# Optimization experiments

Measured on AMD Instinct MI355X. Metric: run time of the kernel, lower is better.

## Reference

```python
import jax, jax.numpy as jnp
import numpy as np

N_GROUPS = 32
N_HEADS = 8
EPS = 1e-5


def group_norm(x, w, b):
    # x: [B, C, T]; GroupNorm32 computes in fp32 then casts back
    B, C, T = x.shape
    xf = x.astype(jnp.float32).reshape(B, N_GROUPS, (C // N_GROUPS) * T)
    mean = xf.mean(axis=-1, keepdims=True)
    var = xf.var(axis=-1, keepdims=True)
    xn = ((xf - mean) * jax.lax.rsqrt(var + EPS)).reshape(B, C, T)
    return (xn * w[None, :, None] + b[None, :, None]).astype(x.dtype)


def attention_block(x, norm_w, norm_b, qkv_w, qkv_b, proj_w, proj_b):
    B, C = x.shape[0], x.shape[1]
    spatial = x.shape[2:]
    xr = x.reshape(B, C, -1)  # [B, C, T]
    T = xr.shape[-1]
    h = group_norm(xr, norm_w, norm_b)
    # 1x1 Conv1d == per-position matmul: [B, 3C, T]
    qkv = jnp.einsum('oc,bct->bot', qkv_w, h) + qkv_b[None, :, None]
    ch = C // N_HEADS  # per-head channels
    q, k, v = jnp.split(qkv, 3, axis=1)
    q = q.reshape(B * N_HEADS, ch, T)
    k = k.reshape(B * N_HEADS, ch, T)
    v = v.reshape(B * N_HEADS, ch, T)
    scale = 1.0 / np.sqrt(ch)
    w = jnp.einsum('bct,bcs->bts', q * scale, k)  # [B*H, T, T]
    w = jax.nn.softmax(w.astype(jnp.float32), axis=-1).astype(w.dtype)
    a = jnp.einsum('bts,bcs->bct', w, v).reshape(B, C, T)
    a = jnp.einsum('oc,bct->bot', proj_w, a) + proj_b[None, :, None]
    return (xr + a).reshape(B, C, *spatial)


def setup_inputs() -> dict:
    key = jax.random.key(0)
    ks = jax.random.split(key, 6)
    B, C, H, W = 16, 512, 32, 32
    return {
        'x': jax.random.normal(ks[0], (B, C, H, W), jnp.float32),
        'norm_w': jnp.ones((C,), jnp.float32),
        'norm_b': jnp.zeros((C,), jnp.float32),
        'qkv_w': jax.random.normal(ks[1], (3 * C, C), jnp.float32) * (1.0 / np.sqrt(C)),
        'qkv_b': jax.random.normal(ks[2], (3 * C,), jnp.float32) * 0.02,
        'proj_w': jax.random.normal(ks[3], (C, C), jnp.float32) * (1.0 / np.sqrt(C)),
        'proj_b': jax.random.normal(ks[4], (C,), jnp.float32) * 0.02,
    }


def reference(x, norm_w, norm_b, qkv_w, qkv_b, proj_w, proj_b):
    return attention_block(x, norm_w, norm_b, qkv_w, qkv_b, proj_w, proj_b)
```

## Files before the change

kernel.cpp:

```cpp
#include <hip/hip_runtime.h>
#include <hip/hip_bf16.h>

#define B_ 16
#define C_ 512
#define T_ 1024
#define G_ 32
#define CPG 16
#define NH 8
#define CH 64
#define EPS 1e-5f

typedef __bf16 bf16x8 __attribute__((ext_vector_type(8)));
typedef __bf16 bf16x4 __attribute__((ext_vector_type(4)));
typedef float f32x4 __attribute__((ext_vector_type(4)));
typedef float f32x16 __attribute__((ext_vector_type(16)));
typedef int i32x4 __attribute__((ext_vector_type(4)));

__device__ __forceinline__ void gload16(const __bf16* g, const __bf16* l) {
    __builtin_amdgcn_global_load_lds(
        (const __attribute__((address_space(1))) unsigned int*)(unsigned long long)(uintptr_t)g,
        (__attribute__((address_space(3))) unsigned int*)(unsigned int)(uintptr_t)l,
        16, 0, 0);
}

__global__ __launch_bounds__(256) void convw_kernel(const float* __restrict__ qw,
                                                    const float* __restrict__ pw,
                                                    __bf16* __restrict__ wqb,
                                                    __bf16* __restrict__ wpb) {
    int idx = (blockIdx.x * 256 + threadIdx.x) * 8;
    const float* src;
    __bf16* dst;
    if (idx < 1536 * 512) { src = qw + idx; dst = wqb + idx; }
    else { src = pw + (idx - 1536 * 512); dst = wpb + (idx - 1536 * 512); }
    float4 a = *(const float4*)src, b = *(const float4*)(src + 4);
    bf16x8 t;
    t[0] = (__bf16)a.x; t[1] = (__bf16)a.y; t[2] = (__bf16)a.z; t[3] = (__bf16)a.w;
    t[4] = (__bf16)b.x; t[5] = (__bf16)b.y; t[6] = (__bf16)b.z; t[7] = (__bf16)b.w;
    *(bf16x8*)dst = t;
}

__global__ __launch_bounds__(256) void gn_kernel(const float* __restrict__ x,
                                                 const float* __restrict__ w,
                                                 const float* __restrict__ bvec,
                                                 __bf16* __restrict__ h_t) {
    const int blk = blockIdx.x;
    const int bb = blk >> 5;
    const int g  = blk & 31;
    const size_t base = ((size_t)bb * C_ + (size_t)g * CPG) * T_;
    const float4* xp = (const float4*)(x + base);
    float4 vals[16];
    float s = 0.f, sq = 0.f;
#pragma unroll
    for (int i = 0; i < 16; ++i) {
        float4 v = xp[threadIdx.x + i * 256];
        vals[i] = v;
        s  += v.x + v.y + v.z + v.w;
        sq += v.x * v.x + v.y * v.y + v.z * v.z + v.w * v.w;
    }
#pragma unroll
    for (int off = 32; off > 0; off >>= 1) {
        s  += __shfl_down(s, off);
        sq += __shfl_down(sq, off);
    }
    __shared__ float red[2][4];
    const int lane = threadIdx.x & 63, wid = threadIdx.x >> 6;
    if (lane == 0) { red[0][wid] = s; red[1][wid] = sq; }
    __syncthreads();
    s  = red[0][0] + red[0][1] + red[0][2] + red[0][3];
    sq = red[1][0] + red[1][1] + red[1][2] + red[1][3];
    const float mean = s * (1.f / 16384.f);
    const float var  = sq * (1.f / 16384.f) - mean * mean;
    const float rstd = rsqrtf(var + EPS);
    float scv[16], shv[16];
#pragma unroll
    for (int i = 0; i < 16; ++i) {
        scv[i] = w[g * CPG + i] * rstd;
        shv[i] = bvec[g * CPG + i] - mean * scv[i];
    }
    __bf16* hb = h_t + ((size_t)bb * T_ + 4 * threadIdx.x) * C_ + g * CPG;
#pragma unroll
    for (int j = 0; j < 4; ++j) {
        bf16x8 t0, t1;
#pragma unroll
        for (int i = 0; i < 8; ++i) {
            float f0 = ((const float*)&vals[i])[j];
            float f1 = ((const float*)&vals[i + 8])[j];
            t0[i] = (__bf16)(f0 * scv[i] + shv[i]);
            t1[i] = (__bf16)(f1 * scv[i + 8] + shv[i + 8]);
        }
        *(bf16x8*)(hb + (size_t)j * C_) = t0;
        *(bf16x8*)(hb + (size_t)j * C_ + 8) = t1;
    }
}

template<int MODE>
__global__ __launch_bounds__(256) void gemm_mfma(const __bf16* __restrict__ Wb,
                                                 const float* __restrict__ bias,
                                                 const __bf16* __restrict__ Bin,
                                                 const float* __restrict__ xres,
                                                 __bf16* __restrict__ qt,
                                                 __bf16* __restrict__ kt,
                                                 __bf16* __restrict__ vb,
                                                 float* __restrict__ outp) {
    __shared__ __align__(16) __bf16 smem[18432];
    __bf16* As = smem;
    __bf16* Bt = smem + 8192;
    const int tid = threadIdx.x, lane = tid & 63, wv = tid >> 6;
    const int wr = wv >> 1, wc = wv & 1, frow = lane & 15, fgrp = lane >> 4;
    const int bz = blockIdx.z, o0 = blockIdx.y << 7, t0 = blockIdx.x << 7;
    const int lrow = lane >> 3, lblk = (lane & 7) ^ (lrow & 7);

    const __bf16* gA = Wb + (size_t)(o0 + wv * 32 + lrow) * 512 + lblk * 8;
    const __bf16* gB = Bin + ((size_t)bz * T_ + t0 + wv * 32 + lrow) * 512 + lblk * 8;
    __bf16* lA = As + wv * 32 * 64;
    __bf16* lB = Bt + wv * 32 * 64;
    const int sb0 = (fgrp ^ (frow & 7)) * 8;
    const int sb1 = ((4 + fgrp) ^ (frow & 7)) * 8;

    f32x4 acc[4][4] = {};
    for (int k0 = 0; k0 < 512; k0 += 64) {
#pragma unroll
        for (int j = 0; j < 4; ++j) {
            gload16(gA + j * 4096 + k0, lA + j * 512);
            gload16(gB + j * 4096 + k0, lB + j * 512);
        }
        __syncthreads();
        bf16x8 af[4][2], bfr[4][2];
#pragma unroll
        for (int m = 0; m < 4; ++m) {
            const __bf16* r = As + (wr * 64 + m * 16 + frow) * 64;
            af[m][0] = *(const bf16x8*)(r + sb0);
            af[m][1] = *(const bf16x8*)(r + sb1);
        }
#pragma unroll
        for (int n = 0; n < 4; ++n) {
            const __bf16* r = Bt + (wc * 64 + n * 16 + frow) * 64;
            bfr[n][0] = *(const bf16x8*)(r + sb0);
            bfr[n][1] = *(const bf16x8*)(r + sb1);
        }
#pragma unroll
        for (int kk = 0; kk < 2; ++kk)
#pragma unroll
            for (int m = 0; m < 4; ++m)
#pragma unroll
                for (int n = 0; n < 4; ++n)
                    acc[m][n] = __builtin_amdgcn_mfma_f32_16x16x32_bf16(af[m][kk], bfr[n][kk], acc[m][n], 0, 0, 0);
        __syncthreads();
    }

    float bias_v[4][4];
#pragma unroll
    for (int m = 0; m < 4; ++m)
#pragma unroll
        for (int r = 0; r < 4; ++r)
            bias_v[m][r] = bias[o0 + wr * 64 + m * 16 + fgrp * 4 + r];

    __bf16* e = smem + wv * 4608;
    if (MODE == 0 && o0 < 1024) {
        const float qsc = (o0 < 512) ? 0.18033688f : 1.0f;
#pragma unroll
        for (int m = 0; m < 4; ++m)
#pragma unroll
            for (int n = 0; n < 4; ++n) {
                bf16x4 v;
#pragma unroll
                for (int r = 0; r < 4; ++r) v[r] = (__bf16)((acc[m][n][r] + bias_v[m][r]) * qsc);
                *(bf16x4*)&e[(n * 16 + frow) * 72 + m * 16 + fgrp * 4] = v;
            }
        __syncthreads();
        __bf16* dst = (o0 < 512) ? qt : kt;
        const int ob = o0 & 511;
#pragma unroll
        for (int p = 0; p < 8; ++p) {
            int row = p * 8 + (lane >> 3), c8 = (lane & 7) * 8;
            *(bf16x8*)(dst + ((size_t)bz * T_ + t0 + wc * 64 + row) * 512 + ob + wr * 64 + c8) =
                *(const bf16x8*)&e[row * 72 + c8];
        }
    } else {
#pragma unroll
        for (int m = 0; m < 4; ++m)
#pragma unroll
            for (int n = 0; n < 4; ++n)
#pragma unroll
                for (int r = 0; r < 4; ++r)
                    e[(m * 16 + fgrp * 4 + r) * 72 + n * 16 + frow] =
                        (__bf16)(acc[m][n][r] + bias_v[m][r]);
        __syncthreads();
        if (MODE == 0) {
            const int ob = o0 - 1024;
#pragma unroll
            for (int p = 0; p < 8; ++p) {
                int row = p * 8 + (lane >> 3), c8 = (lane & 7) * 8;
                *(bf16x8*)(vb + ((size_t)bz * C_ + ob + wr * 64 + row) * T_ + t0 + wc * 64 + c8) =
                    *(const bf16x8*)&e[row * 72 + c8];
            }
        } else {
#pragma unroll
            for (int p = 0; p < 8; ++p) {
                int row = p * 8 + (lane >> 3), c8 = (lane & 7) * 8;
                int o = o0 + wr * 64 + row;
                size_t base = ((size_t)bz * C_ + o) * T_ + t0 + wc * 64 + c8;
                bf16x8 v = *(const bf16x8*)&e[row * 72 + c8];
                float4 x0 = *(const float4*)(xres + base);
                float4 x1 = *(const float4*)(xres + base + 4);
                float4 r0, r1;
                r0.x = x0.x + (float)v[0]; r0.y = x0.y + (float)v[1];
                r0.z = x0.z + (float)v[2]; r0.w = x0.w + (float)v[3];
                r1.x = x1.x + (float)v[4]; r1.y = x1.y + (float)v[5];
                r1.z = x1.z + (float)v[6]; r1.w = x1.w + (float)v[7];
                *(float4*)(outp + base) = r0;
                *(float4*)(outp + base + 4) = r1;
            }
        }
    }
}

__global__ __launch_bounds__(256) void attn32_kernel(const __bf16* __restrict__ qt,
                                                     const __bf16* __restrict__ kt,
                                                     const __bf16* __restrict__ vbuf,
                                                     __bf16* __restrict__ aout) {
    __shared__ __align__(16) __bf16 smem[16384];
    const int tid = threadIdx.x, lane = tid & 63, wv = tid >> 6;
    const int ln = lane & 31, hi = lane >> 5;
    const int lin = blockIdx.y * 8 + blockIdx.x;
    const int work = (lin & 7) * 128 + (lin >> 3);
    const int head = work >> 3;
    const int bb = head >> 3, hh = head & 7;
    const int tq0 = (work & 7) << 7;

    const __bf16* qbase = qt + (size_t)bb * T_ * 512 + hh * CH;
    const __bf16* kbase = kt + (size_t)bb * T_ * 512 + hh * CH;
    const __bf16* vbase = vbuf + ((size_t)bb * C_ + hh * CH) * T_;

    bf16x8 qf[4];
    {
        const __bf16* qr = qbase + (size_t)(tq0 + wv * 32 + ln) * 512 + hi * 8;
#pragma unroll
        for (int st = 0; st < 4; ++st) qf[st] = *(const bf16x8*)(qr + st * 16);
    }

    const int r8 = lane >> 3, cbs = (lane & 7) ^ (lane >> 3);

    f32x16 o0_ = {}, o1_ = {};
    float l = 0.f;

    {
#pragma unroll
        for (int c = 0; c < 2; ++c) {
            int ch = wv * 2 + c;
            gload16(kbase + (size_t)(ch * 8 + r8) * 512 + cbs * 8, smem + ch * 512);
            gload16(vbase + (size_t)(ch * 8 + r8) * T_ + cbs * 8, smem + 4096 + ch * 512);
        }
    }
    __syncthreads();

#pragma unroll 2
    for (int it = 0; it < 16; ++it) {
        const int cur = it & 1;
        if (it < 15) {
            const int s0 = (it + 1) << 6;
            __bf16* base = smem + (cur ^ 1) * 8192;
#pragma unroll
            for (int c = 0; c < 2; ++c) {
                int ch = wv * 2 + c;
                gload16(kbase + (size_t)(s0 + ch * 8 + r8) * 512 + cbs * 8, base + ch * 512);
                gload16(vbase + (size_t)(ch * 8 + r8) * T_ + s0 + cbs * 8, base + 4096 + ch * 512);
            }
        }
        const __bf16* Kb = smem + cur * 8192;
        const __bf16* Vb = Kb + 4096;
        const int rx = ln & 7;

        f32x16 sa0 = {}, sa1 = {};
        {
            const __bf16* kr0 = Kb + (size_t)ln * 64;
            const __bf16* kr1 = Kb + (size_t)(32 + ln) * 64;
            __builtin_amdgcn_s_setprio(1);
#pragma unroll
            for (int st = 0; st < 4; ++st) {
                const int cb = ((hi + 2 * st) ^ rx) << 3;
                bf16x8 k0 = *(const bf16x8*)(kr0 + cb);
                bf16x8 k1 = *(const bf16x8*)(kr1 + cb);
                sa0 = __builtin_amdgcn_mfma_f32_32x32x16_bf16(k0, qf[st], sa0, 0, 0, 0);
                sa1 = __builtin_amdgcn_mfma_f32_32x32x16_bf16(k1, qf[st], sa1, 0, 0, 0);
            }
            __builtin_amdgcn_s_setprio(0);
        }

        float psum0 = 0.f, psum1 = 0.f;
#pragma unroll
        for (int i = 0; i < 16; ++i) {
            sa0[i] = __builtin_amdgcn_exp2f(sa0[i]); psum0 += sa0[i];
        }
#pragma unroll
        for (int i = 0; i < 16; ++i) {
            sa1[i] = __builtin_amdgcn_exp2f(sa1[i]); psum1 += sa1[i];
        }
        l += psum0 + psum1;

        unsigned Wd0[8], Wd1[8];
#pragma unroll
        for (int q = 0; q < 8; ++q) {
            unsigned a0 = (unsigned)__builtin_bit_cast(unsigned short, (__bf16)sa0[2 * q]);
            unsigned a1 = (unsigned)__builtin_bit_cast(unsigned short, (__bf16)sa0[2 * q + 1]);
            Wd0[q] = a0 | (a1 << 16);
            unsigned b0 = (unsigned)__builtin_bit_cast(unsigned short, (__bf16)sa1[2 * q]);
            unsigned b1 = (unsigned)__builtin_bit_cast(unsigned short, (__bf16)sa1[2 * q + 1]);
            Wd1[q] = b0 | (b1 << 16);
        }
        bf16x8 pf[4];
#pragma unroll
        for (int st = 0; st < 4; ++st) {
            const unsigned* W = (st >> 1) ? Wd1 : Wd0;
            const int hf = (st & 1) * 4;
            auto r02 = __builtin_amdgcn_permlane32_swap((int)W[hf + 0], (int)W[hf + 2], false, false);
            auto r13 = __builtin_amdgcn_permlane32_swap((int)W[hf + 1], (int)W[hf + 3], false, false);
            i32x4 pk;
            pk[0] = r02[0]; pk[1] = r13[0]; pk[2] = r02[1]; pk[3] = r13[1];
            pf[st] = __builtin_bit_cast(bf16x8, pk);
        }

        {
            const __bf16* vr0 = Vb + (size_t)ln * 64;
            const __bf16* vr1 = Vb + (size_t)(32 + ln) * 64;
            __builtin_amdgcn_s_setprio(1);
#pragma unroll
            for (int st = 0; st < 4; ++st) {
                const int cb = ((hi + 2 * st) ^ rx) << 3;
                bf16x8 v0 = *(const bf16x8*)(vr0 + cb);
                bf16x8 v1 = *(const bf16x8*)(vr1 + cb);
                o0_ = __builtin_amdgcn_mfma_f32_32x32x16_bf16(v0, pf[st], o0_, 0, 0, 0);
                o1_ = __builtin_amdgcn_mfma_f32_32x32x16_bf16(v1, pf[st], o1_, 0, 0, 0);
            }
            __builtin_amdgcn_s_setprio(0);
        }
        __syncthreads();
    }

    l += __shfl_xor(l, 32);
    const float rl = 1.f / l;
    __bf16* e = smem + wv * 2304;
#pragma unroll
    for (int ct = 0; ct < 2; ++ct) {
        const f32x16& oc = ct ? o1_ : o0_;
#pragma unroll
        for (int q = 0; q < 8; ++q) {
            int c0 = ct * 32 + 2 * (q & 1) + 8 * (q >> 1) + 4 * hi;
            unsigned u0 = (unsigned)__builtin_bit_cast(unsigned short, (__bf16)(oc[2 * q] * rl));
            unsigned u1 = (unsigned)__builtin_bit_cast(unsigned short, (__bf16)(oc[2 * q + 1] * rl));
            *(unsigned*)&e[(size_t)ln * 72 + c0] = u0 | (u1 << 16);
        }
    }
    __syncthreads();
    {
        const int t = lane >> 1, chalf = lane & 1;
        __bf16* dst = aout + ((size_t)bb * T_ + tq0 + wv * 32 + t) * 512 + hh * CH + chalf * 32;
        const __bf16* er = e + t * 72 + chalf * 32;
#pragma unroll
        for (int k = 0; k < 4; ++k)
            *(bf16x8*)(dst + k * 8) = *(const bf16x8*)(er + k * 8);
    }
}

extern "C" void kernel_launch(void* const* d_in, const int* in_sizes, int n_in,
                              void* d_out, int out_size, void* d_ws, size_t ws_size,
                              hipStream_t stream) {
    const float* x      = (const float*)d_in[0];
    const float* norm_w = (const float*)d_in[1];
    const float* norm_b = (const float*)d_in[2];
    const float* qkv_w  = (const float*)d_in[3];
    const float* qkv_b  = (const float*)d_in[4];
    const float* proj_w = (const float*)d_in[5];
    const float* proj_b = (const float*)d_in[6];
    float* out = (float*)d_out;

    __bf16* h_t = (__bf16*)d_ws;
    __bf16* wqb = h_t + (size_t)8388608;
    __bf16* wpb = wqb + 786432;
    __bf16* qt  = wpb + 262144;
    __bf16* kt  = qt + (size_t)8388608;
    __bf16* vb  = kt + (size_t)8388608;
    __bf16* at  = vb + (size_t)8388608;

    convw_kernel<<<512, 256, 0, stream>>>(qkv_w, proj_w, wqb, wpb);
    gn_kernel<<<512, 256, 0, stream>>>(x, norm_w, norm_b, h_t);
    gemm_mfma<0><<<dim3(8, 12, 16), 256, 0, stream>>>(wqb, qkv_b, h_t, nullptr, qt, kt, vb, nullptr);
    attn32_kernel<<<dim3(8, 128), 256, 0, stream>>>(qt, kt, vb, at);
    gemm_mfma<1><<<dim3(8, 4, 16), 256, 0, stream>>>(wpb, proj_b, at, x, nullptr, nullptr, nullptr, out);
}
```

Measured before the change: 123.0 us.

## Double query rows per wave in attention to reuse K/V tiles

Each wave now handles 64 query rows (two 32-row subtiles) instead of 32, so a block covers 256 queries and the grid shrinks from 1024 to 512 blocks. Each K and V fragment read from LDS feeds twice as many MFMAs, and K/V global traffic per query is halved. The cost is double the accumulator and score registers, which pressures occupancy, and fewer blocks on the GPU. Launch bounds are set to 2 blocks per CU and the epilogue staging buffer is enlarged to hold 256 rows.

Result: faster. 116.6 us (-5.2%).

```diff
diff --git a/kernel.cpp b/kernel.cpp
--- a/kernel.cpp
+++ b/kernel.cpp
@@ -215,42 +215,42 @@
     }
 }
 
-__global__ __launch_bounds__(256) void attn32_kernel(const __bf16* __restrict__ qt,
-                                                     const __bf16* __restrict__ kt,
-                                                     const __bf16* __restrict__ vbuf,
-                                                     __bf16* __restrict__ aout) {
-    __shared__ __align__(16) __bf16 smem[16384];
+__global__ __launch_bounds__(256, 2) void attn32_kernel(const __bf16* __restrict__ qt,
+                                                        const __bf16* __restrict__ kt,
+                                                        const __bf16* __restrict__ vbuf,
+                                                        __bf16* __restrict__ aout) {
+    __shared__ __align__(16) __bf16 smem[18432];
     const int tid = threadIdx.x, lane = tid & 63, wv = tid >> 6;
     const int ln = lane & 31, hi = lane >> 5;
-    const int lin = blockIdx.y * 8 + blockIdx.x;
-    const int work = (lin & 7) * 128 + (lin >> 3);
-    const int head = work >> 3;
+    const int lin = blockIdx.x;
+    const int work = (lin & 7) * 64 + (lin >> 3);
+    const int head = work >> 2;
     const int bb = head >> 3, hh = head & 7;
-    const int tq0 = (work & 7) << 7;
+    const int tq0 = (work & 3) << 8;
 
     const __bf16* qbase = qt + (size_t)bb * T_ * 512 + hh * CH;
     const __bf16* kbase = kt + (size_t)bb * T_ * 512 + hh * CH;
     const __bf16* vbase = vbuf + ((size_t)bb * C_ + hh * CH) * T_;
 
-    bf16x8 qf[4];
-    {
-        const __bf16* qr = qbase + (size_t)(tq0 + wv * 32 + ln) * 512 + hi * 8;
-#pragma unroll
-        for (int st = 0; st < 4; ++st) qf[st] = *(const bf16x8*)(qr + st * 16);
+    bf16x8 qf[2][4];
+#pragma unroll
+    for (int sub = 0; sub < 2; ++sub) {
+        const __bf16* qr = qbase + (size_t)(tq0 + wv * 64 + sub * 32 + ln) * 512 + hi * 8;
+#pragma unroll
+        for (int st = 0; st < 4; ++st) qf[sub][st] = *(const bf16x8*)(qr + st * 16);
     }
 
     const int r8 = lane >> 3, cbs = (lane & 7) ^ (lane >> 3);
-
-    f32x16 o0_ = {}, o1_ = {};
-    float l = 0.f;
-
-    {
-#pragma unroll
-        for (int c = 0; c < 2; ++c) {
-            int ch = wv * 2 + c;
-            gload16(kbase + (size_t)(ch * 8 + r8) * 512 + cbs * 8, smem + ch * 512);
-            gload16(vbase + (size_t)(ch * 8 + r8) * T_ + cbs * 8, smem + 4096 + ch * 512);
-        }
+    const int rx = ln & 7;
+
+    f32x16 o00 = {}, o01 = {}, o10 = {}, o11 = {};
+    float l0 = 0.f, l1 = 0.f;
+
+#pragma unroll
+    for (int c = 0; c < 2; ++c) {
+        int ch = wv * 2 + c;
+        gload16(kbase + (size_t)(ch * 8 + r8) * 512 + cbs * 8, smem + ch * 512);
+        gload16(vbase + (size_t)(ch * 8 + r8) * T_ + cbs * 8, smem + 4096 + ch * 512);
     }
     __syncthreads();
 
@@ -258,106 +258,118 @@
     for (int it = 0; it < 16; ++it) {
         const int cur = it & 1;
         if (it < 15) {
-            const int s0 = (it + 1) << 6;
+            const int s0n = (it + 1) << 6;
             __bf16* base = smem + (cur ^ 1) * 8192;
 #pragma unroll
             for (int c = 0; c < 2; ++c) {
                 int ch = wv * 2 + c;
-                gload16(kbase + (size_t)(s0 + ch * 8 + r8) * 512 + cbs * 8, base + ch * 512);
-                gload16(vbase + (size_t)(ch * 8 + r8) * T_ + s0 + cbs * 8, base + 4096 + ch * 512);
+                gload16(kbase + (size_t)(s0n + ch * 8 + r8) * 512 + cbs * 8, base + ch * 512);
+                gload16(vbase + (size_t)(ch * 8 + r8) * T_ + s0n + cbs * 8, base + 4096 + ch * 512);
             }
         }
         const __bf16* Kb = smem + cur * 8192;
         const __bf16* Vb = Kb + 4096;
-        const int rx = ln & 7;
-
-        f32x16 sa0 = {}, sa1 = {};
+
+        f32x16 sa00 = {}, sa01 = {}, sa10 = {}, sa11 = {};
         {
-            const __bf16* kr0 = Kb + (size_t)ln * 64;
-            const __bf16* kr1 = Kb + (size_t)(32 + ln) * 64;
             __builtin_amdgcn_s_setprio(1);
 #pragma unroll
             for (int st = 0; st < 4; ++st) {
                 const int cb = ((hi + 2 * st) ^ rx) << 3;
-                bf16x8 k0 = *(const bf16x8*)(kr0 + cb);
-                bf16x8 k1 = *(const bf16x8*)(kr1 + cb);
-                sa0 = __builtin_amdgcn_mfma_f32_32x32x16_bf16(k0, qf[st], sa0, 0, 0, 0);
-                sa1 = __builtin_amdgcn_mfma_f32_32x32x16_bf16(k1, qf[st], sa1, 0, 0, 0);
+                bf16x8 k0 = *(const bf16x8*)(Kb + (size_t)ln * 64 + cb);
+                bf16x8 k1 = *(const bf16x8*)(Kb + (size_t)(32 + ln) * 64 + cb);
+                sa00 = __builtin_amdgcn_mfma_f32_32x32x16_bf16(k0, qf[0][st], sa00, 0, 0, 0);
+                sa01 = __builtin_amdgcn_mfma_f32_32x32x16_bf16(k1, qf[0][st], sa01, 0, 0, 0);
+                sa10 = __builtin_amdgcn_mfma_f32_32x32x16_bf16(k0, qf[1][st], sa10, 0, 0, 0);
+                sa11 = __builtin_amdgcn_mfma_f32_32x32x16_bf16(k1, qf[1][st], sa11, 0, 0, 0);
             }
             __builtin_amdgcn_s_setprio(0);
         }
 
-        float psum0 = 0.f, psum1 = 0.f;
-#pragma unroll
-        for (int i = 0; i < 16; ++i) {
-            sa0[i] = __builtin_amdgcn_exp2f(sa0[i]); psum0 += sa0[i];
-        }
-#pragma unroll
-        for (int i = 0; i < 16; ++i) {
-            sa1[i] = __builtin_amdgcn_exp2f(sa1[i]); psum1 += sa1[i];
-        }
-        l += psum0 + psum1;
-
-        unsigned Wd0[8], Wd1[8];
-#pragma unroll
-        for (int q = 0; q < 8; ++q) {
-            unsigned a0 = (unsigned)__builtin_bit_cast(unsigned short, (__bf16)sa0[2 * q]);
-            unsigned a1 = (unsigned)__builtin_bit_cast(unsigned short, (__bf16)sa0[2 * q + 1]);
-            Wd0[q] = a0 | (a1 << 16);
-            unsigned b0 = (unsigned)__builtin_bit_cast(unsigned short, (__bf16)sa1[2 * q]);
-            unsigned b1 = (unsigned)__builtin_bit_cast(unsigned short, (__bf16)sa1[2 * q + 1]);
-            Wd1[q] = b0 | (b1 << 16);
-        }
-        bf16x8 pf[4];
-#pragma unroll
-        for (int st = 0; st < 4; ++st) {
-            const unsigned* W = (st >> 1) ? Wd1 : Wd0;
-            const int hf = (st & 1) * 4;
-            auto r02 = __builtin_amdgcn_permlane32_swap((int)W[hf + 0], (int)W[hf + 2], false, false);
-            auto r13 = __builtin_amdgcn_permlane32_swap((int)W[hf + 1], (int)W[hf + 3], false, false);
-            i32x4 pk;
-            pk[0] = r02[0]; pk[1] = r13[0]; pk[2] = r02[1]; pk[3] = r13[1];
-            pf[st] = __builtin_bit_cast(bf16x8, pk);
+        float pa = 0.f, pb = 0.f, pc = 0.f, pd = 0.f;
+#pragma unroll
+        for (int i = 0; i < 16; ++i) { sa00[i] = __builtin_amdgcn_exp2f(sa00[i]); pa += sa00[i]; }
+#pragma unroll
+        for (int i = 0; i < 16; ++i) { sa01[i] = __builtin_amdgcn_exp2f(sa01[i]); pb += sa01[i]; }
+#pragma unroll
+        for (int i = 0; i < 16; ++i) { sa10[i] = __builtin_amdgcn_exp2f(sa10[i]); pc += sa10[i]; }
+#pragma unroll
+        for (int i = 0; i < 16; ++i) { sa11[i] = __builtin_amdgcn_exp2f(sa11[i]); pd += sa11[i]; }
+        l0 += pa + pb;
+        l1 += pc + pd;
+
+        bf16x8 pfA[4], pfB[4];
+#pragma unroll
+        for (int sub = 0; sub < 2; ++sub) {
+            const f32x16& s_lo = sub ? sa10 : sa00;
+            const f32x16& s_hi = sub ? sa11 : sa01;
+            unsigned Wd0[8], Wd1[8];
+#pragma unroll
+            for (int q = 0; q < 8; ++q) {
+                unsigned a0 = (unsigned)__builtin_bit_cast(unsigned short, (__bf16)s_lo[2 * q]);
+                unsigned a1 = (unsigned)__builtin_bit_cast(unsigned short, (__bf16)s_lo[2 * q + 1]);
+                Wd0[q] = a0 | (a1 << 16);
+                unsigned b0 = (unsigned)__builtin_bit_cast(unsigned short, (__bf16)s_hi[2 * q]);
+                unsigned b1 = (unsigned)__builtin_bit_cast(unsigned short, (__bf16)s_hi[2 * q + 1]);
+                Wd1[q] = b0 | (b1 << 16);
+            }
+            bf16x8* pf = sub ? pfB : pfA;
+#pragma unroll
+            for (int st = 0; st < 4; ++st) {
+                const unsigned* W = (st >> 1) ? Wd1 : Wd0;
+                const int hf = (st & 1) * 4;
+                auto r02 = __builtin_amdgcn_permlane32_swap((int)W[hf + 0], (int)W[hf + 2], false, false);
+                auto r13 = __builtin_amdgcn_permlane32_swap((int)W[hf + 1], (int)W[hf + 3], false, false);
+                i32x4 pk;
+                pk[0] = r02[0]; pk[1] = r13[0]; pk[2] = r02[1]; pk[3] = r13[1];
+                pf[st] = __builtin_bit_cast(bf16x8, pk);
+            }
         }
 
         {
-            const __bf16* vr0 = Vb + (size_t)ln * 64;
-            const __bf16* vr1 = Vb + (size_t)(32 + ln) * 64;
             __builtin_amdgcn_s_setprio(1);
 #pragma unroll
             for (int st = 0; st < 4; ++st) {
                 const int cb = ((hi + 2 * st) ^ rx) << 3;
-                bf16x8 v0 = *(const bf16x8*)(vr0 + cb);
-                bf16x8 v1 = *(const bf16x8*)(vr1 + cb);
-                o0_ = __builtin_amdgcn_mfma_f32_32x32x16_bf16(v0, pf[st], o0_, 0, 0, 0);
-                o1_ = __builtin_amdgcn_mfma_f32_32x32x16_bf16(v1, pf[st], o1_, 0, 0, 0);
+                bf16x8 v0 = *(const bf16x8*)(Vb + (size_t)ln * 64 + cb);
+                bf16x8 v1 = *(const bf16x8*)(Vb + (size_t)(32 + ln) * 64 + cb);
+                o00 = __builtin_amdgcn_mfma_f32_32x32x16_bf16(v0, pfA[st], o00, 0, 0, 0);
+                o01 = __builtin_amdgcn_mfma_f32_32x32x16_bf16(v1, pfA[st], o01, 0, 0, 0);
+                o10 = __builtin_amdgcn_mfma_f32_32x32x16_bf16(v0, pfB[st], o10, 0, 0, 0);
+                o11 = __builtin_amdgcn_mfma_f32_32x32x16_bf16(v1, pfB[st], o11, 0, 0, 0);
             }
             __builtin_amdgcn_s_setprio(0);
         }
         __syncthreads();
     }
 
-    l += __shfl_xor(l, 32);
-    const float rl = 1.f / l;
-    __bf16* e = smem + wv * 2304;
-#pragma unroll
-    for (int ct = 0; ct < 2; ++ct) {
-        const f32x16& oc = ct ? o1_ : o0_;
-#pragma unroll
-        for (int q = 0; q < 8; ++q) {
-            int c0 = ct * 32 + 2 * (q & 1) + 8 * (q >> 1) + 4 * hi;
-            unsigned u0 = (unsigned)__builtin_bit_cast(unsigned short, (__bf16)(oc[2 * q] * rl));
-            unsigned u1 = (unsigned)__builtin_bit_cast(unsigned short, (__bf16)(oc[2 * q + 1] * rl));
-            *(unsigned*)&e[(size_t)ln * 72 + c0] = u0 | (u1 << 16);
+    l0 += __shfl_xor(l0, 32);
+    l1 += __shfl_xor(l1, 32);
+    const float rl0 = 1.f / l0, rl1 = 1.f / l1;
+    __bf16* e = smem;
+#pragma unroll
+    for (int sub = 0; sub < 2; ++sub) {
+        const float rl = sub ? rl1 : rl0;
+        const int row = wv * 64 + sub * 32 + ln;
+#pragma unroll
+        for (int ct = 0; ct < 2; ++ct) {
+            const f32x16& oc = sub ? (ct ? o11 : o10) : (ct ? o01 : o00);
+#pragma unroll
+            for (int q = 0; q < 8; ++q) {
+                int c0 = ct * 32 + 2 * (q & 1) + 8 * (q >> 1) + 4 * hi;
+                unsigned u0 = (unsigned)__builtin_bit_cast(unsigned short, (__bf16)(oc[2 * q] * rl));
+                unsigned u1 = (unsigned)__builtin_bit_cast(unsigned short, (__bf16)(oc[2 * q + 1] * rl));
+                *(unsigned*)&e[(size_t)row * 72 + c0] = u0 | (u1 << 16);
+            }
         }
     }
     __syncthreads();
     {
-        const int t = lane >> 1, chalf = lane & 1;
-        __bf16* dst = aout + ((size_t)bb * T_ + tq0 + wv * 32 + t) * 512 + hh * CH + chalf * 32;
-        const __bf16* er = e + t * 72 + chalf * 32;
-#pragma unroll
-        for (int k = 0; k < 4; ++k)
+        const int r = tid;
+        __bf16* dst = aout + ((size_t)bb * T_ + tq0 + r) * 512 + hh * CH;
+        const __bf16* er = e + (size_t)r * 72;
+#pragma unroll
+        for (int k = 0; k < 8; ++k)
             *(bf16x8*)(dst + k * 8) = *(const bf16x8*)(er + k * 8);
     }
 }
@@ -385,6 +397,6 @@
     convw_kernel<<<512, 256, 0, stream>>>(qkv_w, proj_w, wqb, wpb);
     gn_kernel<<<512, 256, 0, stream>>>(x, norm_w, norm_b, h_t);
     gemm_mfma<0><<<dim3(8, 12, 16), 256, 0, stream>>>(wqb, qkv_b, h_t, nullptr, qt, kt, vb, nullptr);
-    attn32_kernel<<<dim3(8, 128), 256, 0, stream>>>(qt, kt, vb, at);
+    attn32_kernel<<<dim3(512), 256, 0, stream>>>(qt, kt, vb, at);
     gemm_mfma<1><<<dim3(8, 4, 16), 256, 0, stream>>>(wpb, proj_b, at, x, nullptr, nullptr, nullptr, out);
 }
```
